# Kernel tuning notes

Measured on AMD Instinct MI355X. Metric: run time of the kernel, lower is better.

Reference implementation:

```python
import jax, jax.numpy as jnp
import numpy as np

N = 1_048_576      # flattened batch (forward reshapes to (-1, 4))
Q_DIM = 4
HIDDEN = 64
DC = Q_DIM // 2    # q_dim_changed = 2
NUM_LO = (DC * DC - DC) // 2  # = 1
SLOPE = 0.01       # torch leaky_relu default negative slope


def setup_inputs() -> dict:
    key = jax.random.key(0)
    ks = jax.random.split(key, 9)
    def lin(kw, kb, fan_out, fan_in):
        bound = 1.0 / np.sqrt(fan_in)
        W = jax.random.uniform(kw, (fan_out, fan_in), jnp.float32, -bound, bound)
        b = jax.random.uniform(kb, (fan_out,), jnp.float32, -bound, bound)
        return W, b
    x = jax.random.normal(ks[0], (N, Q_DIM), jnp.float32)
    W1, b1 = lin(ks[1], ks[2], HIDDEN, Q_DIM)
    W2, b2 = lin(ks[3], ks[4], HIDDEN, HIDDEN)
    W_Ld, b_Ld = lin(ks[5], ks[6], DC, HIDDEN)
    W_Lo, b_Lo = lin(ks[7], ks[8], NUM_LO, HIDDEN)
    return {"x": x, "W1": W1, "b1": b1, "W2": W2, "b2": b2,
            "W_Ld": W_Ld, "b_Ld": b_Ld, "W_Lo": W_Lo, "b_Lo": b_Lo}


def reference(x, W1, b1, W2, b2, W_Ld, b_Ld, W_Lo, b_Lo):
    q = x.reshape(-1, Q_DIM)                      # (n, 4)
    n = q.shape[0]
    h1 = jax.nn.leaky_relu(q @ W1.T + b1, SLOPE)  # (n, 64)
    h2 = jax.nn.leaky_relu(h1 @ W2.T + b2, SLOPE) # (n, 64); dropout is eval-mode identity
    Ld = jax.nn.softplus(h2 @ W_Ld.T + b_Ld)      # (n, 2) positive diagonal
    Lo = h2 @ W_Lo.T + b_Lo                       # (n, 1) strictly-lower entries
    rows, cols = jnp.tril_indices(DC, -1)         # strictly lower triangle, row-major
    diag = jnp.arange(DC)
    L = jnp.zeros((n, DC, DC), dtype=q.dtype)
    L = L.at[:, rows, cols].set(Lo)               # scatter Lo (matches torch boolean-mask fill order)
    L = L.at[:, diag, diag].set(Ld)               # diag_embed(Ld)
    H = jnp.einsum('nij,nkj->nik', L, L) + 1e-9 * jnp.eye(DC, dtype=q.dtype)
    return H
```

## Files before the change

kernel.cpp:

```cpp
#include <hip/hip_runtime.h>


typedef __attribute__((ext_vector_type(8))) short bf16x8;
typedef __attribute__((ext_vector_type(4))) float f32x4;

#define ROWS_PER_BLOCK 256
#define H_STRIDE 72
#define LDS_SHORTS (ROWS_PER_BLOCK * H_STRIDE)

__device__ __forceinline__ float lrelu(float a) {
    return fmaxf(a, 0.01f * a);
}

__device__ __forceinline__ float softplus(float v) {
    return fmaxf(v, 0.0f) + log1pf(expf(-fabsf(v)));
}

__device__ __forceinline__ unsigned short bf16_rne(float f) {
    unsigned u = __float_as_uint(f);
    u += 0x7FFFu + ((u >> 16) & 1u);
    return (unsigned short)(u >> 16);
}

__device__ __forceinline__ unsigned pk_bf16(float lo, float hi) {
    return (unsigned)bf16_rne(lo) | ((unsigned)bf16_rne(hi) << 16);
}

__global__ __launch_bounds__(256) void dln_mfma(
    const float* __restrict__ x,
    const float* __restrict__ W1,  const float* __restrict__ b1,
    const float* __restrict__ W2,  const float* __restrict__ b2,
    const float* __restrict__ WLd, const float* __restrict__ bLd,
    const float* __restrict__ WLo, const float* __restrict__ bLo,
    float* __restrict__ out)
{
    __shared__ __align__(16) unsigned short lds[LDS_SHORTS];

    const int tid  = threadIdx.x;
    const int lane = tid & 63;
    const int wv   = tid >> 6;
    const int quad = lane >> 4;
    const int col  = lane & 15;

    {
        const float4* src = (const float4*)W2;
        float4*       dst = (float4*)lds;
#pragma unroll
        for (int i = 0; i < 4; ++i)
            dst[tid + 256 * i] = src[tid + 256 * i];
    }
    float b2c[4];
#pragma unroll
    for (int t = 0; t < 4; ++t) b2c[t] = b2[16 * t + col];
    __syncthreads();

    bf16x8 bfrag[4][2];
    {
        const float* w2l = (const float*)lds;
#pragma unroll
        for (int t = 0; t < 4; ++t) {
#pragma unroll
            for (int s = 0; s < 2; ++s) {
                const float* p = w2l + (16 * t + col) * 64 + 32 * s + 8 * quad;
                float4 f0 = *(const float4*)(p);
                float4 f1 = *(const float4*)(p + 4);
                uint4 u;
                u.x = pk_bf16(f0.x, f0.y);
                u.y = pk_bf16(f0.z, f0.w);
                u.z = pk_bf16(f1.x, f1.y);
                u.w = pk_bf16(f1.z, f1.w);
                bfrag[t][s] = __builtin_bit_cast(bf16x8, u);
            }
        }
    }
    __syncthreads();

    const int row_g = blockIdx.x * ROWS_PER_BLOCK + tid;
    {
        const float4 qv = ((const float4*)x)[row_g];
        unsigned short* myrow = lds + tid * H_STRIDE;
#pragma unroll
        for (int blk = 0; blk < 8; ++blk) {
            unsigned up[4];
#pragma unroll
            for (int p = 0; p < 4; ++p) {
                float h[2];
#pragma unroll
                for (int e = 0; e < 2; ++e) {
                    const int j = blk * 8 + p * 2 + e;
                    float a = b1[j];
                    a = fmaf(qv.x, W1[4 * j + 0], a);
                    a = fmaf(qv.y, W1[4 * j + 1], a);
                    a = fmaf(qv.z, W1[4 * j + 2], a);
                    a = fmaf(qv.w, W1[4 * j + 3], a);
                    h[e] = lrelu(a);
                }
                up[p] = pk_bf16(h[0], h[1]);
            }
            *(uint4*)(myrow + blk * 8) = make_uint4(up[0], up[1], up[2], up[3]);
        }
    }

#pragma unroll
    for (int mt = 0; mt < 4; ++mt) {
        const int rbase = wv * 64 + mt * 16;
        const unsigned short* ar = lds + (rbase + col) * H_STRIDE + 8 * quad;
        uint4 a0u = *(const uint4*)(ar);
        uint4 a1u = *(const uint4*)(ar + 32);
        bf16x8 a0 = __builtin_bit_cast(bf16x8, a0u);
        bf16x8 a1 = __builtin_bit_cast(bf16x8, a1u);

        f32x4 acc[4];
#pragma unroll
        for (int t = 0; t < 4; ++t) {
            acc[t] = (f32x4){b2c[t], b2c[t], b2c[t], b2c[t]};
            acc[t] = __builtin_amdgcn_mfma_f32_16x16x32_bf16(a0, bfrag[t][0], acc[t], 0, 0, 0);
            acc[t] = __builtin_amdgcn_mfma_f32_16x16x32_bf16(a1, bfrag[t][1], acc[t], 0, 0, 0);
        }
#pragma unroll
        for (int t = 0; t < 4; ++t) {
#pragma unroll
            for (int r = 0; r < 4; ++r) {
                const float v = lrelu(acc[t][r]);
                lds[(rbase + quad * 4 + r) * H_STRIDE + 16 * t + col] = bf16_rne(v);
            }
        }
    }
    __syncthreads();

    {
        const unsigned short* hr = lds + tid * H_STRIDE;
        float ld0 = bLd[0];
        float ld1 = bLd[1];
        float lo  = bLo[0];
#pragma unroll
        for (int i = 0; i < 8; ++i) {
            const uint4 u = *(const uint4*)(hr + i * 8);
            const unsigned uu[4] = {u.x, u.y, u.z, u.w};
#pragma unroll
            for (int p = 0; p < 4; ++p) {
                const int k = i * 8 + p * 2;
                const float e0 = __uint_as_float(uu[p] << 16);
                const float e1 = __uint_as_float(uu[p] & 0xFFFF0000u);
                ld0 = fmaf(e0, WLd[k],          ld0);
                ld0 = fmaf(e1, WLd[k + 1],      ld0);
                ld1 = fmaf(e0, WLd[64 + k],     ld1);
                ld1 = fmaf(e1, WLd[64 + k + 1], ld1);
                lo  = fmaf(e0, WLo[k],          lo);
                lo  = fmaf(e1, WLo[k + 1],      lo);
            }
        }
        ld0 = softplus(ld0);
        ld1 = softplus(ld1);
        float4 o;
        o.x = fmaf(ld0, ld0, 1e-9f);
        o.y = ld0 * lo;
        o.z = o.y;
        o.w = fmaf(lo, lo, fmaf(ld1, ld1, 1e-9f));
        reinterpret_cast<float4*>(out)[row_g] = o;
    }
}

__global__ __launch_bounds__(256) void dln_tail(
    const float* __restrict__ x,
    const float* __restrict__ W1,  const float* __restrict__ b1,
    const float* __restrict__ W2,  const float* __restrict__ b2,
    const float* __restrict__ WLd, const float* __restrict__ bLd,
    const float* __restrict__ WLo, const float* __restrict__ bLo,
    float* __restrict__ out, int row0, int nrows)
{
    const int row = row0 + blockIdx.x * 256 + threadIdx.x;
    if (row >= nrows) return;
    const float4 qv = reinterpret_cast<const float4*>(x)[row];
    float h1[64];
#pragma unroll
    for (int j = 0; j < 64; ++j) {
        float a = b1[j];
        a = fmaf(qv.x, W1[4 * j + 0], a);
        a = fmaf(qv.y, W1[4 * j + 1], a);
        a = fmaf(qv.z, W1[4 * j + 2], a);
        a = fmaf(qv.w, W1[4 * j + 3], a);
        h1[j] = lrelu(a);
    }
    float ld0 = bLd[0], ld1 = bLd[1], lo = bLo[0];
#pragma unroll 4
    for (int j = 0; j < 64; ++j) {
        float a0 = b2[j], a1 = 0.0f;
        const float* w = W2 + 64 * j;
#pragma unroll
        for (int k = 0; k < 64; k += 2) {
            a0 = fmaf(h1[k],     w[k],     a0);
            a1 = fmaf(h1[k + 1], w[k + 1], a1);
        }
        const float a = lrelu(a0 + a1);
        ld0 = fmaf(a, WLd[j],      ld0);
        ld1 = fmaf(a, WLd[64 + j], ld1);
        lo  = fmaf(a, WLo[j],      lo);
    }
    ld0 = softplus(ld0);
    ld1 = softplus(ld1);
    float4 o;
    o.x = fmaf(ld0, ld0, 1e-9f);
    o.y = ld0 * lo;
    o.z = o.y;
    o.w = fmaf(lo, lo, fmaf(ld1, ld1, 1e-9f));
    reinterpret_cast<float4*>(out)[row] = o;
}

extern "C" void kernel_launch(void* const* d_in, const int* in_sizes, int n_in,
                              void* d_out, int out_size, void* d_ws, size_t ws_size,
                              hipStream_t stream)
{
    const float* x   = (const float*)d_in[0];
    const float* W1  = (const float*)d_in[1];
    const float* b1  = (const float*)d_in[2];
    const float* W2  = (const float*)d_in[3];
    const float* b2  = (const float*)d_in[4];
    const float* WLd = (const float*)d_in[5];
    const float* bLd = (const float*)d_in[6];
    const float* WLo = (const float*)d_in[7];
    const float* bLo = (const float*)d_in[8];
    float* out = (float*)d_out;

    const int nrows = in_sizes[0] / 4;
    const int nfull = nrows / ROWS_PER_BLOCK;
    const int rem   = nrows - nfull * ROWS_PER_BLOCK;

    if (nfull > 0)
        dln_mfma<<<nfull, 256, 0, stream>>>(
            x, W1, b1, W2, b2, WLd, bLd, WLo, bLo, out);
    if (rem > 0)
        dln_tail<<<(rem + 255) / 256, 256, 0, stream>>>(
            x, W1, b1, W2, b2, WLd, bLd, WLo, bLo, out,
            nfull * ROWS_PER_BLOCK, nrows);
}
```

Measured before the change: 130.7 us.

## Keep MLP activations in registers and reduce output heads via cross-lane shuffles

Layer 1 is now computed directly in the MFMA A-fragment layout, and the small output heads are reduced from the MFMA accumulators with 16-lane xor shuffles. This removes the large LDS staging buffer and the block-wide barriers between stages. W2 fragments are read straight from global memory instead of being staged through LDS, and W1/b1 are cached in a small LDS array. The cost is extra shuffle work, and only 4 of 16 lanes issue the final store, so stores are less coalesced.

```diff
diff --git a/kernel.cpp b/kernel.cpp
--- a/kernel.cpp
+++ b/kernel.cpp
@@ -5,8 +5,6 @@
 typedef __attribute__((ext_vector_type(4))) float f32x4;
 
 #define ROWS_PER_BLOCK 256
-#define H_STRIDE 72
-#define LDS_SHORTS (ROWS_PER_BLOCK * H_STRIDE)
 
 __device__ __forceinline__ float lrelu(float a) {
     return fmaxf(a, 0.01f * a);
@@ -24,6 +22,12 @@
 
 __device__ __forceinline__ unsigned pk_bf16(float lo, float hi) {
     return (unsigned)bf16_rne(lo) | ((unsigned)bf16_rne(hi) << 16);
+}
+
+__device__ __forceinline__ float sel4(const float h[4], int c) {
+    const float a = (c & 1) ? h[1] : h[0];
+    const float b = (c & 1) ? h[3] : h[2];
+    return (c & 2) ? b : a;
 }
 
 __global__ __launch_bounds__(256) void dln_mfma(
@@ -34,7 +38,8 @@
     const float* __restrict__ WLo, const float* __restrict__ bLo,
     float* __restrict__ out)
 {
-    __shared__ __align__(16) unsigned short lds[LDS_SHORTS];
+    __shared__ __align__(16) float w1s[256];
+    __shared__ float b1s[64];
 
     const int tid  = threadIdx.x;
     const int lane = tid & 63;
@@ -42,73 +47,70 @@
     const int quad = lane >> 4;
     const int col  = lane & 15;
 
-    {
-        const float4* src = (const float4*)W2;
-        float4*       dst = (float4*)lds;
-#pragma unroll
-        for (int i = 0; i < 4; ++i)
-            dst[tid + 256 * i] = src[tid + 256 * i];
-    }
-    float b2c[4];
-#pragma unroll
-    for (int t = 0; t < 4; ++t) b2c[t] = b2[16 * t + col];
+    w1s[tid] = W1[tid];
+    if (tid < 64) b1s[tid] = b1[tid];
+
+    float wld0[4], wld1[4], wlo[4], b2c[4];
+#pragma unroll
+    for (int t = 0; t < 4; ++t) {
+        const int n = 16 * t + col;
+        wld0[t] = WLd[n];
+        wld1[t] = WLd[64 + n];
+        wlo[t]  = WLo[n];
+        b2c[t]  = b2[n];
+    }
+    const float bld0 = bLd[0], bld1 = bLd[1], blo = bLo[0];
+
+    bf16x8 bfrag[4][2];
+#pragma unroll
+    for (int t = 0; t < 4; ++t) {
+#pragma unroll
+        for (int s = 0; s < 2; ++s) {
+            const float* p = W2 + (16 * t + col) * 64 + 32 * s + 8 * quad;
+            const float4 f0 = *(const float4*)(p);
+            const float4 f1 = *(const float4*)(p + 4);
+            uint4 u;
+            u.x = pk_bf16(f0.x, f0.y);
+            u.y = pk_bf16(f0.z, f0.w);
+            u.z = pk_bf16(f1.x, f1.y);
+            u.w = pk_bf16(f1.z, f1.w);
+            bfrag[t][s] = __builtin_bit_cast(bf16x8, u);
+        }
+    }
+
     __syncthreads();
 
-    bf16x8 bfrag[4][2];
-    {
-        const float* w2l = (const float*)lds;
-#pragma unroll
-        for (int t = 0; t < 4; ++t) {
-#pragma unroll
-            for (int s = 0; s < 2; ++s) {
-                const float* p = w2l + (16 * t + col) * 64 + 32 * s + 8 * quad;
-                float4 f0 = *(const float4*)(p);
-                float4 f1 = *(const float4*)(p + 4);
-                uint4 u;
-                u.x = pk_bf16(f0.x, f0.y);
-                u.y = pk_bf16(f0.z, f0.w);
-                u.z = pk_bf16(f1.x, f1.y);
-                u.w = pk_bf16(f1.z, f1.w);
-                bfrag[t][s] = __builtin_bit_cast(bf16x8, u);
-            }
-        }
-    }
-    __syncthreads();
-
-    const int row_g = blockIdx.x * ROWS_PER_BLOCK + tid;
-    {
-        const float4 qv = ((const float4*)x)[row_g];
-        unsigned short* myrow = lds + tid * H_STRIDE;
-#pragma unroll
-        for (int blk = 0; blk < 8; ++blk) {
-            unsigned up[4];
-#pragma unroll
-            for (int p = 0; p < 4; ++p) {
+    const int base = blockIdx.x * ROWS_PER_BLOCK + wv * 64;
+
+#pragma unroll
+    for (int mt = 0; mt < 4; ++mt) {
+        const int rbase = base + mt * 16;
+
+        const float4 q = ((const float4*)x)[rbase + col];
+
+        unsigned au[8];
+#pragma unroll
+        for (int s = 0; s < 2; ++s) {
+#pragma unroll
+            for (int jj = 0; jj < 4; ++jj) {
+                const int k0 = 32 * s + 8 * quad + 2 * jj;
                 float h[2];
 #pragma unroll
                 for (int e = 0; e < 2; ++e) {
-                    const int j = blk * 8 + p * 2 + e;
-                    float a = b1[j];
-                    a = fmaf(qv.x, W1[4 * j + 0], a);
-                    a = fmaf(qv.y, W1[4 * j + 1], a);
-                    a = fmaf(qv.z, W1[4 * j + 2], a);
-                    a = fmaf(qv.w, W1[4 * j + 3], a);
+                    const int k = k0 + e;
+                    const float4 w = *(const float4*)(w1s + 4 * k);
+                    float a = b1s[k];
+                    a = fmaf(q.x, w.x, a);
+                    a = fmaf(q.y, w.y, a);
+                    a = fmaf(q.z, w.z, a);
+                    a = fmaf(q.w, w.w, a);
                     h[e] = lrelu(a);
                 }
-                up[p] = pk_bf16(h[0], h[1]);
+                au[s * 4 + jj] = pk_bf16(h[0], h[1]);
             }
-            *(uint4*)(myrow + blk * 8) = make_uint4(up[0], up[1], up[2], up[3]);
-        }
-    }
-
-#pragma unroll
-    for (int mt = 0; mt < 4; ++mt) {
-        const int rbase = wv * 64 + mt * 16;
-        const unsigned short* ar = lds + (rbase + col) * H_STRIDE + 8 * quad;
-        uint4 a0u = *(const uint4*)(ar);
-        uint4 a1u = *(const uint4*)(ar + 32);
-        bf16x8 a0 = __builtin_bit_cast(bf16x8, a0u);
-        bf16x8 a1 = __builtin_bit_cast(bf16x8, a1u);
+        }
+        const bf16x8 a0 = __builtin_bit_cast(bf16x8, make_uint4(au[0], au[1], au[2], au[3]));
+        const bf16x8 a1 = __builtin_bit_cast(bf16x8, make_uint4(au[4], au[5], au[6], au[7]));
 
         f32x4 acc[4];
 #pragma unroll
@@ -117,47 +119,39 @@
             acc[t] = __builtin_amdgcn_mfma_f32_16x16x32_bf16(a0, bfrag[t][0], acc[t], 0, 0, 0);
             acc[t] = __builtin_amdgcn_mfma_f32_16x16x32_bf16(a1, bfrag[t][1], acc[t], 0, 0, 0);
         }
-#pragma unroll
-        for (int t = 0; t < 4; ++t) {
+
+        float hd0[4], hd1[4], hdo[4];
+#pragma unroll
+        for (int r = 0; r < 4; ++r) {
+            const float l0 = lrelu(acc[0][r]);
+            const float l1 = lrelu(acc[1][r]);
+            const float l2 = lrelu(acc[2][r]);
+            const float l3 = lrelu(acc[3][r]);
+            hd0[r] = fmaf(l3, wld0[3], fmaf(l2, wld0[2], fmaf(l1, wld0[1], l0 * wld0[0])));
+            hd1[r] = fmaf(l3, wld1[3], fmaf(l2, wld1[2], fmaf(l1, wld1[1], l0 * wld1[0])));
+            hdo[r] = fmaf(l3, wlo[3],  fmaf(l2, wlo[2],  fmaf(l1, wlo[1],  l0 * wlo[0])));
+        }
+#pragma unroll
+        for (int m = 1; m < 16; m <<= 1) {
 #pragma unroll
             for (int r = 0; r < 4; ++r) {
-                const float v = lrelu(acc[t][r]);
-                lds[(rbase + quad * 4 + r) * H_STRIDE + 16 * t + col] = bf16_rne(v);
+                hd0[r] += __shfl_xor(hd0[r], m, 16);
+                hd1[r] += __shfl_xor(hd1[r], m, 16);
+                hdo[r] += __shfl_xor(hdo[r], m, 16);
             }
         }
-    }
-    __syncthreads();
-
-    {
-        const unsigned short* hr = lds + tid * H_STRIDE;
-        float ld0 = bLd[0];
-        float ld1 = bLd[1];
-        float lo  = bLo[0];
-#pragma unroll
-        for (int i = 0; i < 8; ++i) {
-            const uint4 u = *(const uint4*)(hr + i * 8);
-            const unsigned uu[4] = {u.x, u.y, u.z, u.w};
-#pragma unroll
-            for (int p = 0; p < 4; ++p) {
-                const int k = i * 8 + p * 2;
-                const float e0 = __uint_as_float(uu[p] << 16);
-                const float e1 = __uint_as_float(uu[p] & 0xFFFF0000u);
-                ld0 = fmaf(e0, WLd[k],          ld0);
-                ld0 = fmaf(e1, WLd[k + 1],      ld0);
-                ld1 = fmaf(e0, WLd[64 + k],     ld1);
-                ld1 = fmaf(e1, WLd[64 + k + 1], ld1);
-                lo  = fmaf(e0, WLo[k],          lo);
-                lo  = fmaf(e1, WLo[k + 1],      lo);
-            }
-        }
-        ld0 = softplus(ld0);
-        ld1 = softplus(ld1);
-        float4 o;
-        o.x = fmaf(ld0, ld0, 1e-9f);
-        o.y = ld0 * lo;
-        o.z = o.y;
-        o.w = fmaf(lo, lo, fmaf(ld1, ld1, 1e-9f));
-        reinterpret_cast<float4*>(out)[row_g] = o;
+
+        if (col < 4) {
+            const float ld0 = softplus(sel4(hd0, col) + bld0);
+            const float ld1 = softplus(sel4(hd1, col) + bld1);
+            const float lo  = sel4(hdo, col) + blo;
+            float4 o;
+            o.x = fmaf(ld0, ld0, 1e-9f);
+            o.y = ld0 * lo;
+            o.z = o.y;
+            o.w = fmaf(lo, lo, fmaf(ld1, ld1, 1e-9f));
+            reinterpret_cast<float4*>(out)[rbase + quad * 4 + col] = o;
+        }
     }
 }
 
```

After: 203.1 us. 1.55x slower.
